# Kernel tuning notes

Measured on AMD Instinct MI355X. Metric: run time of the kernel, lower is better.

Reference implementation:

```python
import jax, jax.numpy as jnp
import numpy as np

N = 100000   # nodes
E = 1600000  # edges (avg degree 16)
D = 64       # input_dim == hidden_dim
EPS = 1e-5


def setup_inputs() -> dict:
    key = jax.random.key(0)
    ks = jax.random.split(key, 6)
    x = jax.random.normal(ks[0], (N, D), dtype=jnp.float32)
    edge_index = jax.random.randint(ks[1], (2, E), 0, N, dtype=jnp.int32)
    edge_feature = jax.random.uniform(ks[2], (E,), dtype=jnp.float32)
    scale = 1.0 / np.sqrt(D)
    W1 = jax.random.normal(ks[3], (D, D), dtype=jnp.float32) * scale
    b1 = jnp.zeros((D,), jnp.float32)
    gamma = jnp.ones((D,), jnp.float32)
    beta = jnp.zeros((D,), jnp.float32)
    W2 = jax.random.normal(ks[4], (D, D), dtype=jnp.float32) * scale
    b2 = jnp.zeros((D,), jnp.float32)
    return {"x": x, "edge_index": edge_index, "edge_feature": edge_feature,
            "W1": W1, "b1": b1, "gamma": gamma, "beta": beta, "W2": W2, "b2": b2}


def _gcn_conv(x, W, b, src, dst, edge_weight, n):
    # PyG GCNConv: h = X W; add self-loops (weight 1); sym-normalize; scatter-add; + bias
    h = x @ W                                    # [N, D]
    loop = jnp.arange(n, dtype=src.dtype)
    s = jnp.concatenate([src, loop])             # [E+N]
    d = jnp.concatenate([dst, loop])
    w = jnp.concatenate([edge_weight, jnp.ones((n,), x.dtype)])
    deg = jax.ops.segment_sum(w, d, num_segments=n)          # in-degree (weighted)
    dinv = jnp.where(deg > 0, jax.lax.rsqrt(deg), 0.0)
    norm = dinv[s] * w * dinv[d]                 # [E+N]
    msg = h[s] * norm[:, None]                   # gather + scale
    out = jax.ops.segment_sum(msg, d, num_segments=n)        # scatter-add at target
    return out + b


def reference(x, edge_index, edge_feature, W1, b1, gamma, beta, W2, b2):
    src, dst = edge_index[0], edge_index[1]
    n = x.shape[0]
    h = _gcn_conv(x, W1, b1, src, dst, edge_feature, n)
    # BatchNorm1d in training mode: batch stats over the node dimension
    mu = jnp.mean(h, axis=0)
    var = jnp.var(h, axis=0)
    h = gamma * (h - mu) * jax.lax.rsqrt(var + EPS) + beta
    h = jax.nn.relu(h)                           # dropout p=0.0 -> identity
    return _gcn_conv(h, W2, b2, src, dst, edge_feature, n)
```

## Files before the change

kernel.cpp:

```cpp
#include <hip/hip_runtime.h>

#define D 64
#define EPS 1e-5f
#define FP_SCALE 1099511627776.0f

static __device__ __forceinline__ unsigned f2bf(float f) {
    unsigned u = __float_as_uint(f);
    unsigned r = ((u >> 16) & 1u) + 0x7fffu;
    return (u + r) >> 16;
}

__global__ void k_init(unsigned long long* __restrict__ packed,
                       float* __restrict__ stats, int n) {
    int i = blockIdx.x * 256 + threadIdx.x;
    if (i < n) packed[i] = 0ull;
    if (i < 128) stats[i] = 0.0f;
}

__global__ void k_cnt(const int* __restrict__ dst, const float* __restrict__ w,
                      unsigned long long* __restrict__ packed,
                      int* __restrict__ rank, int E) {
    int e = blockIdx.x * 256 + threadIdx.x;
    if (e < E) {
        unsigned long long v = (1ull << 52) |
            (unsigned long long)(w[e] * FP_SCALE);
        unsigned long long old = atomicAdd(&packed[dst[e]], v);
        rank[e] = (int)(old >> 52);
    }
}

__global__ void k_deg(const unsigned long long* __restrict__ packed,
                      float* __restrict__ dinv, int n) {
    int i = blockIdx.x * 256 + threadIdx.x;
    if (i < n) {
        float wsum = (float)(packed[i] & ((1ull << 52) - 1ull)) * (1.0f / FP_SCALE);
        dinv[i] = rsqrtf(1.0f + wsum);
    }
}

__global__ void k_scan1(const unsigned long long* __restrict__ packed,
                        int* __restrict__ incl, int* __restrict__ bsum, int n) {
    __shared__ int sm[256];
    int i = blockIdx.x * 256 + threadIdx.x;
    int v = (i < n) ? (int)(packed[i] >> 52) : 0;
    sm[threadIdx.x] = v;
    __syncthreads();
    for (int off = 1; off < 256; off <<= 1) {
        int t = 0;
        if (threadIdx.x >= off) t = sm[threadIdx.x - off];
        __syncthreads();
        if (threadIdx.x >= off) sm[threadIdx.x] += t;
        __syncthreads();
    }
    if (i < n) incl[i] = sm[threadIdx.x];
    if (threadIdx.x == 255) bsum[blockIdx.x] = sm[255];
}

__global__ void k_scan2(int* __restrict__ bsum, int nb) {
    __shared__ int sm[512];
    int v = (threadIdx.x < nb) ? bsum[threadIdx.x] : 0;
    sm[threadIdx.x] = v;
    __syncthreads();
    for (int off = 1; off < 512; off <<= 1) {
        int t = 0;
        if (threadIdx.x >= off) t = sm[threadIdx.x - off];
        __syncthreads();
        if (threadIdx.x >= off) sm[threadIdx.x] += t;
        __syncthreads();
    }
    if (threadIdx.x < nb) bsum[threadIdx.x] = sm[threadIdx.x] - v;
}

__global__ void k_scan3(const unsigned long long* __restrict__ packed,
                        const int* __restrict__ incl, const int* __restrict__ boff,
                        int* __restrict__ rowptr, int n, int E) {
    int i = blockIdx.x * 256 + threadIdx.x;
    if (i < n) {
        int c = (int)(packed[i] >> 52);
        rowptr[i] = incl[i] - c + boff[blockIdx.x];
        if (i == n - 1) rowptr[n] = E;
    }
}

__global__ void k_fill(const int* __restrict__ src, const int* __restrict__ dst,
                       const float* __restrict__ w, const float* __restrict__ dinv,
                       const int* __restrict__ rowptr, const int* __restrict__ rank,
                       float2* __restrict__ edata, int E) {
    int e = blockIdx.x * 256 + threadIdx.x;
    if (e < E) {
        int s = src[e], d = dst[e];
        edata[rowptr[d] + rank[e]] =
            make_float2(__int_as_float(s), dinv[s] * w[e] * dinv[d]);
    }
}

template <bool BN>
__global__ void k_gemm(const float* __restrict__ x, const float* __restrict__ W,
                       const float* __restrict__ stats, unsigned* __restrict__ outb,
                       int n) {
    __shared__ float Wl[D][D];
    __shared__ float xs[8][D];
    int tid = threadIdx.x;
    int l   = tid & 31;
    int ns  = tid >> 5;
    for (int t = tid; t < D * D; t += 256) Wl[t >> 6][t & 63] = W[t];
    __syncthreads();
    for (int base = blockIdx.x * 8; base < n; base += gridDim.x * 8) {
        __syncthreads();
        for (int t = tid; t < 8 * D; t += 256) {
            int r = t >> 6, c = t & 63;
            int node = base + r;
            float v = 0.f;
            if (node < n) {
                v = x[node * D + c];
                if (BN) v = fmaxf(fmaf(v, stats[c], stats[64 + c]), 0.f);
            }
            xs[r][c] = v;
        }
        __syncthreads();
        int node = base + ns;
        if (node < n) {
            float a0 = 0.f, a1 = 0.f;
#pragma unroll
            for (int k = 0; k < D; ++k) {
                float xv  = xs[ns][k];
                float2 wp = ((const float2*)Wl[k])[l];
                a0 = fmaf(xv, wp.x, a0);
                a1 = fmaf(xv, wp.y, a1);
            }
            outb[node * 32 + l] = f2bf(a0) | (f2bf(a1) << 16);
        }
    }
}

template <bool STATS>
__global__ void k_agg(const unsigned* __restrict__ hb, const float2* __restrict__ edata,
                      const int* __restrict__ rowptr, const float* __restrict__ dinv,
                      const float* __restrict__ bias, float* __restrict__ out,
                      float* __restrict__ stats, int n) {
    float2* op = (float2*)out;
    int tid  = threadIdx.x;
    int wv   = tid >> 6;
    int lane = tid & 63;
    int half = lane >> 5;
    int l    = lane & 31;
    float2 bb = make_float2(0.f, 0.f);
    if (bias) bb = ((const float2*)bias)[l];
    float2 s = make_float2(0.f, 0.f), q = make_float2(0.f, 0.f);

    for (int d0 = blockIdx.x * 8; d0 < n; d0 += gridDim.x * 8) {
        int d = d0 + wv * 2 + half;
        if (d < n) {
            float di = dinv[d];
            float sl = di * di;
            unsigned vs = hb[d * 32 + l];
            float2 acc;
            acc.x = fmaf(__uint_as_float(vs << 16),          sl, bb.x);
            acc.y = fmaf(__uint_as_float(vs & 0xffff0000u),  sl, bb.y);
            int k  = rowptr[d];
            int k1 = rowptr[d + 1];
            for (; k + 4 <= k1; k += 4) {
                float2 m0 = edata[k + 0];
                float2 m1 = edata[k + 1];
                float2 m2 = edata[k + 2];
                float2 m3 = edata[k + 3];
                unsigned v0 = hb[__float_as_int(m0.x) * 32 + l];
                unsigned v1 = hb[__float_as_int(m1.x) * 32 + l];
                unsigned v2 = hb[__float_as_int(m2.x) * 32 + l];
                unsigned v3 = hb[__float_as_int(m3.x) * 32 + l];
                acc.x = fmaf(__uint_as_float(v0 << 16),         m0.y, acc.x);
                acc.y = fmaf(__uint_as_float(v0 & 0xffff0000u), m0.y, acc.y);
                acc.x = fmaf(__uint_as_float(v1 << 16),         m1.y, acc.x);
                acc.y = fmaf(__uint_as_float(v1 & 0xffff0000u), m1.y, acc.y);
                acc.x = fmaf(__uint_as_float(v2 << 16),         m2.y, acc.x);
                acc.y = fmaf(__uint_as_float(v2 & 0xffff0000u), m2.y, acc.y);
                acc.x = fmaf(__uint_as_float(v3 << 16),         m3.y, acc.x);
                acc.y = fmaf(__uint_as_float(v3 & 0xffff0000u), m3.y, acc.y);
            }
            for (; k < k1; ++k) {
                float2 m = edata[k];
                unsigned v = hb[__float_as_int(m.x) * 32 + l];
                acc.x = fmaf(__uint_as_float(v << 16),         m.y, acc.x);
                acc.y = fmaf(__uint_as_float(v & 0xffff0000u), m.y, acc.y);
            }
            op[d * 32 + l] = acc;
            if (STATS) {
                s.x += acc.x; s.y += acc.y;
                q.x = fmaf(acc.x, acc.x, q.x);
                q.y = fmaf(acc.y, acc.y, q.y);
            }
        }
    }
    if (STATS) {
        __shared__ float2 ls[4][2][32];
        __shared__ float2 lq[4][2][32];
        ls[wv][half][l] = s;
        lq[wv][half][l] = q;
        __syncthreads();
        if (tid < 32) {
            float2 S = make_float2(0.f, 0.f), Q = make_float2(0.f, 0.f);
#pragma unroll
            for (int w2 = 0; w2 < 4; ++w2)
#pragma unroll
                for (int hh = 0; hh < 2; ++hh) {
                    S.x += ls[w2][hh][tid].x; S.y += ls[w2][hh][tid].y;
                    Q.x += lq[w2][hh][tid].x; Q.y += lq[w2][hh][tid].y;
                }
            atomicAdd(&stats[2 * tid],     S.x);
            atomicAdd(&stats[2 * tid + 1], S.y);
            atomicAdd(&stats[64 + 2 * tid],     Q.x);
            atomicAdd(&stats[64 + 2 * tid + 1], Q.y);
        }
    }
}

__global__ void k_finalize(float* __restrict__ stats, const float* __restrict__ gamma,
                           const float* __restrict__ beta, float inv_n) {
    int j = threadIdx.x;
    if (j < 64) {
        float mean = stats[j] * inv_n;
        float var  = stats[64 + j] * inv_n - mean * mean;
        float sc   = gamma[j] * rsqrtf(var + EPS);
        stats[j]      = sc;
        stats[64 + j] = beta[j] - mean * sc;
    }
}

extern "C" void kernel_launch(void* const* d_in, const int* in_sizes, int n_in,
                              void* d_out, int out_size, void* d_ws, size_t ws_size,
                              hipStream_t stream) {
    const float* x     = (const float*)d_in[0];
    const int*   ei    = (const int*)d_in[1];
    const float* ew    = (const float*)d_in[2];
    const float* W1    = (const float*)d_in[3];
    const float* gamma = (const float*)d_in[5];
    const float* beta  = (const float*)d_in[6];
    const float* W2    = (const float*)d_in[7];
    const float* b2    = (const float*)d_in[8];
    float*       out   = (float*)d_out;

    const int N = in_sizes[0] / D;
    const int E = in_sizes[2];
    const int* src = ei;
    const int* dst = ei + E;

    float2*             edata  = (float2*)d_ws;
    unsigned long long* packed = (unsigned long long*)(edata + E);
    unsigned*           hb     = (unsigned*)(packed + N);
    float*              agg1   = (float*)(hb + (size_t)N * 32);
    float*              dinv   = agg1 + (size_t)N * D;
    float*              stats  = dinv + N;
    int*                rowptr = (int*)(stats + 128);
    int*                tmp    = rowptr + N + 1;
    int*                rank   = tmp + N;
    int*                bsum   = rank + E;

    const int nb_n = (N + 255) / 256;
    const int nb_e = (E + 255) / 256;

    k_init<<<nb_n, 256, 0, stream>>>(packed, stats, N);
    k_cnt<<<nb_e, 256, 0, stream>>>(dst, ew, packed, rank, E);
    k_deg<<<nb_n, 256, 0, stream>>>(packed, dinv, N);

    k_scan1<<<nb_n, 256, 0, stream>>>(packed, tmp, bsum, N);
    k_scan2<<<1, 512, 0, stream>>>(bsum, nb_n);
    k_scan3<<<nb_n, 256, 0, stream>>>(packed, tmp, bsum, rowptr, N, E);
    k_fill<<<nb_e, 256, 0, stream>>>(src, dst, ew, dinv, rowptr, rank, edata, E);

    k_gemm<false><<<2048, 256, 0, stream>>>(x, W1, nullptr, hb, N);
    k_agg<true><<<2048, 256, 0, stream>>>(hb, edata, rowptr, dinv, nullptr, agg1, stats, N);
    k_finalize<<<1, 64, 0, stream>>>(stats, gamma, beta, 1.0f / (float)N);

    k_gemm<true><<<2048, 256, 0, stream>>>(agg1, W2, stats, hb, N);
    k_agg<false><<<2048, 256, 0, stream>>>(hb, edata, rowptr, dinv, b2, out, nullptr, N);
}
```

Before: 469.3 us.

## Aggregate 8 nodes per wavefront with 16-byte bf16 gathers

Reworks the CSR aggregation kernel so each wavefront processes 8 destination nodes, with 8 lanes per node each loading a uint4 (8 bf16 features) per neighbor, instead of 2 nodes per wave with 4-byte loads. The grid now has one block per 32 nodes instead of a grid-stride loop. BatchNorm statistics are reduced with cross-lane shuffles before the shared-memory and atomic step. This aims to raise memory-level parallelism and cut the number of gather instructions. In exchange, lanes idle when degrees differ within a wave, and the kernel issues many more atomics because there are far more blocks.

```diff
diff --git a/kernel.cpp b/kernel.cpp
--- a/kernel.cpp
+++ b/kernel.cpp
@@ -133,83 +133,89 @@
     }
 }
 
+#define ACC8(v, wgt)                                                  \
+    acc[0] = fmaf(__uint_as_float((v).x << 16),         (wgt), acc[0]); \
+    acc[1] = fmaf(__uint_as_float((v).x & 0xffff0000u), (wgt), acc[1]); \
+    acc[2] = fmaf(__uint_as_float((v).y << 16),         (wgt), acc[2]); \
+    acc[3] = fmaf(__uint_as_float((v).y & 0xffff0000u), (wgt), acc[3]); \
+    acc[4] = fmaf(__uint_as_float((v).z << 16),         (wgt), acc[4]); \
+    acc[5] = fmaf(__uint_as_float((v).z & 0xffff0000u), (wgt), acc[5]); \
+    acc[6] = fmaf(__uint_as_float((v).w << 16),         (wgt), acc[6]); \
+    acc[7] = fmaf(__uint_as_float((v).w & 0xffff0000u), (wgt), acc[7]);
+
 template <bool STATS>
-__global__ void k_agg(const unsigned* __restrict__ hb, const float2* __restrict__ edata,
+__global__ void k_agg(const uint4* __restrict__ hb4, const float2* __restrict__ edata,
                       const int* __restrict__ rowptr, const float* __restrict__ dinv,
                       const float* __restrict__ bias, float* __restrict__ out,
                       float* __restrict__ stats, int n) {
-    float2* op = (float2*)out;
     int tid  = threadIdx.x;
     int wv   = tid >> 6;
     int lane = tid & 63;
-    int half = lane >> 5;
-    int l    = lane & 31;
-    float2 bb = make_float2(0.f, 0.f);
-    if (bias) bb = ((const float2*)bias)[l];
-    float2 s = make_float2(0.f, 0.f), q = make_float2(0.f, 0.f);
-
-    for (int d0 = blockIdx.x * 8; d0 < n; d0 += gridDim.x * 8) {
-        int d = d0 + wv * 2 + half;
-        if (d < n) {
-            float di = dinv[d];
-            float sl = di * di;
-            unsigned vs = hb[d * 32 + l];
-            float2 acc;
-            acc.x = fmaf(__uint_as_float(vs << 16),          sl, bb.x);
-            acc.y = fmaf(__uint_as_float(vs & 0xffff0000u),  sl, bb.y);
-            int k  = rowptr[d];
-            int k1 = rowptr[d + 1];
-            for (; k + 4 <= k1; k += 4) {
-                float2 m0 = edata[k + 0];
-                float2 m1 = edata[k + 1];
-                float2 m2 = edata[k + 2];
-                float2 m3 = edata[k + 3];
-                unsigned v0 = hb[__float_as_int(m0.x) * 32 + l];
-                unsigned v1 = hb[__float_as_int(m1.x) * 32 + l];
-                unsigned v2 = hb[__float_as_int(m2.x) * 32 + l];
-                unsigned v3 = hb[__float_as_int(m3.x) * 32 + l];
-                acc.x = fmaf(__uint_as_float(v0 << 16),         m0.y, acc.x);
-                acc.y = fmaf(__uint_as_float(v0 & 0xffff0000u), m0.y, acc.y);
-                acc.x = fmaf(__uint_as_float(v1 << 16),         m1.y, acc.x);
-                acc.y = fmaf(__uint_as_float(v1 & 0xffff0000u), m1.y, acc.y);
-                acc.x = fmaf(__uint_as_float(v2 << 16),         m2.y, acc.x);
-                acc.y = fmaf(__uint_as_float(v2 & 0xffff0000u), m2.y, acc.y);
-                acc.x = fmaf(__uint_as_float(v3 << 16),         m3.y, acc.x);
-                acc.y = fmaf(__uint_as_float(v3 & 0xffff0000u), m3.y, acc.y);
+    int slot = lane >> 3;
+    int c    = lane & 7;
+    int d    = blockIdx.x * 32 + wv * 8 + slot;
+
+    float acc[8] = {0.f, 0.f, 0.f, 0.f, 0.f, 0.f, 0.f, 0.f};
+    int k = 0, k1 = 0;
+    if (d < n) { k = rowptr[d]; k1 = rowptr[d + 1]; }
+
+    while (__any(k < k1)) {
+        bool a0 = k < k1;
+        bool a1 = k + 1 < k1;
+        float2 m0, m1;
+        uint4  v0, v1;
+        if (a0) { m0 = edata[k];     v0 = hb4[__float_as_int(m0.x) * 8 + c]; }
+        if (a1) { m1 = edata[k + 1]; v1 = hb4[__float_as_int(m1.x) * 8 + c]; }
+        if (a0) { ACC8(v0, m0.y) }
+        if (a1) { ACC8(v1, m1.y) }
+        k += 2;
+    }
+
+    if (d < n) {
+        float di = dinv[d];
+        float sl = di * di;
+        uint4 vs = hb4[d * 8 + c];
+        ACC8(vs, sl)
+        if (bias) {
+            float4 b0 = ((const float4*)bias)[2 * c];
+            float4 b1 = ((const float4*)bias)[2 * c + 1];
+            acc[0] += b0.x; acc[1] += b0.y; acc[2] += b0.z; acc[3] += b0.w;
+            acc[4] += b1.x; acc[5] += b1.y; acc[6] += b1.z; acc[7] += b1.w;
+        }
+        float4* op = (float4*)out;
+        op[d * 16 + 2 * c]     = make_float4(acc[0], acc[1], acc[2], acc[3]);
+        op[d * 16 + 2 * c + 1] = make_float4(acc[4], acc[5], acc[6], acc[7]);
+    }
+
+    if (STATS) {
+        float s[8], q[8];
+#pragma unroll
+        for (int i = 0; i < 8; ++i) {
+            float a = (d < n) ? acc[i] : 0.f;
+            s[i] = a;
+            q[i] = a * a;
+        }
+#pragma unroll
+        for (int m = 8; m <= 32; m <<= 1) {
+#pragma unroll
+            for (int i = 0; i < 8; ++i) {
+                s[i] += __shfl_xor(s[i], m);
+                q[i] += __shfl_xor(q[i], m);
             }
-            for (; k < k1; ++k) {
-                float2 m = edata[k];
-                unsigned v = hb[__float_as_int(m.x) * 32 + l];
-                acc.x = fmaf(__uint_as_float(v << 16),         m.y, acc.x);
-                acc.y = fmaf(__uint_as_float(v & 0xffff0000u), m.y, acc.y);
-            }
-            op[d * 32 + l] = acc;
-            if (STATS) {
-                s.x += acc.x; s.y += acc.y;
-                q.x = fmaf(acc.x, acc.x, q.x);
-                q.y = fmaf(acc.y, acc.y, q.y);
-            }
-        }
-    }
-    if (STATS) {
-        __shared__ float2 ls[4][2][32];
-        __shared__ float2 lq[4][2][32];
-        ls[wv][half][l] = s;
-        lq[wv][half][l] = q;
-        __syncthreads();
-        if (tid < 32) {
-            float2 S = make_float2(0.f, 0.f), Q = make_float2(0.f, 0.f);
-#pragma unroll
-            for (int w2 = 0; w2 < 4; ++w2)
-#pragma unroll
-                for (int hh = 0; hh < 2; ++hh) {
-                    S.x += ls[w2][hh][tid].x; S.y += ls[w2][hh][tid].y;
-                    Q.x += lq[w2][hh][tid].x; Q.y += lq[w2][hh][tid].y;
-                }
-            atomicAdd(&stats[2 * tid],     S.x);
-            atomicAdd(&stats[2 * tid + 1], S.y);
-            atomicAdd(&stats[64 + 2 * tid],     Q.x);
-            atomicAdd(&stats[64 + 2 * tid + 1], Q.y);
+        }
+        __shared__ float ls[4][8][8];
+        __shared__ float lq[4][8][8];
+        if (slot == 0) {
+#pragma unroll
+            for (int i = 0; i < 8; ++i) { ls[wv][c][i] = s[i]; lq[wv][c][i] = q[i]; }
+        }
+        __syncthreads();
+        if (tid < 64) {
+            int cc = tid >> 3, r = tid & 7;
+            float S = ls[0][cc][r] + ls[1][cc][r] + ls[2][cc][r] + ls[3][cc][r];
+            float Q = lq[0][cc][r] + lq[1][cc][r] + lq[2][cc][r] + lq[3][cc][r];
+            atomicAdd(&stats[8 * cc + r],      S);
+            atomicAdd(&stats[64 + 8 * cc + r], Q);
         }
     }
 }
@@ -257,6 +263,7 @@
 
     const int nb_n = (N + 255) / 256;
     const int nb_e = (E + 255) / 256;
+    const int nb_a = (N + 31) / 32;
 
     k_init<<<nb_n, 256, 0, stream>>>(packed, stats, N);
     k_cnt<<<nb_e, 256, 0, stream>>>(dst, ew, packed, rank, E);
@@ -268,9 +275,11 @@
     k_fill<<<nb_e, 256, 0, stream>>>(src, dst, ew, dinv, rowptr, rank, edata, E);
 
     k_gemm<false><<<2048, 256, 0, stream>>>(x, W1, nullptr, hb, N);
-    k_agg<true><<<2048, 256, 0, stream>>>(hb, edata, rowptr, dinv, nullptr, agg1, stats, N);
+    k_agg<true><<<nb_a, 256, 0, stream>>>((const uint4*)hb, edata, rowptr, dinv,
+                                          nullptr, agg1, stats, N);
     k_finalize<<<1, 64, 0, stream>>>(stats, gamma, beta, 1.0f / (float)N);
 
     k_gemm<true><<<2048, 256, 0, stream>>>(agg1, W2, stats, hb, N);
-    k_agg<false><<<2048, 256, 0, stream>>>(hb, edata, rowptr, dinv, b2, out, nullptr, N);
-}
+    k_agg<false><<<nb_a, 256, 0, stream>>>((const uint4*)hb, edata, rowptr, dinv,
+                                           b2, out, nullptr, N);
+}
```

Result: faster. 422.1 us (-10.1%).
